# Kernel tuning notes

Measured on AMD Instinct MI355X. Metric: run time of the kernel, lower is better.

The kernel has to match this reference:

```python
import jax, jax.numpy as jnp
import numpy as np

B, L, D, H1, OUT, MAX_W = 16, 128, 768, 770, 40, 30


def _span_mask():
    # valid spans: i <= j and width < MAX_W (structured sparsity over the L x L grid)
    ii, jj = np.meshgrid(np.arange(L), np.arange(L), indexing='ij')
    return ((jj >= ii) & (jj - ii < MAX_W)).astype(np.int32)


def setup_inputs():
    key = jax.random.key(0)
    ks = jax.random.split(key, 5)
    hidden_states = jax.random.normal(ks[0], (B, L + 1, D), dtype=jnp.float32)
    rng = np.random.default_rng(0)
    starts = rng.integers(0, L - MAX_W, size=(B,))
    ends = starts + rng.integers(0, MAX_W, size=(B,))
    pred_spans = jnp.asarray(np.stack([starts, ends], axis=1), dtype=jnp.int32)
    span_mask = jnp.asarray(_span_mask())
    W1 = 0.02 * jax.random.normal(ks[1], (2 * D + 1, H1), dtype=jnp.float32)
    b1 = jax.random.normal(ks[2], (H1,), dtype=jnp.float32)
    W2 = 0.02 * jax.random.normal(ks[3], (H1, OUT), dtype=jnp.float32)
    b2 = jax.random.normal(ks[4], (OUT,), dtype=jnp.float32)
    return dict(hidden_states=hidden_states, pred_spans=pred_spans, token_num=L,
                span_available_indication_matrix=span_mask,
                W1=W1, b1=b1, W2=W2, b2=b2)


def reference(hidden_states, pred_spans, token_num, span_available_indication_matrix, W1, b1, W2, b2):
    # span mask is an integer constant -> resolve valid (i, j) pairs on host
    mask = np.asarray(span_available_indication_matrix)
    vi, vj = np.nonzero(mask == 1)            # [n_valid] each
    vi_j = jnp.asarray(vi)
    vj_j = jnp.asarray(vj)
    vecs = hidden_states[:, 1:token_num + 1, :]  # token t -> hidden[:, t+1, :], [B, L, D]
    xi = vecs[:, vi_j, :]                        # [B, n_valid, D] gather of span-start vecs
    xj = vecs[:, vj_j, :]                        # [B, n_valid, D] gather of span-end vecs
    # pred_indications: 2 if span == pred span; 1 if strictly inside it (i<=j); else 0
    s = pred_spans[:, 0:1]
    e = pred_spans[:, 1:2]
    i_ = vi_j[None, :]
    j_ = vj_j[None, :]
    exact = (i_ == s) & (j_ == e)
    inside = (i_ >= s) & (j_ <= e) & (i_ <= j_)
    ind = jnp.where(exact, 2.0, jnp.where(inside, 1.0, 0.0)).astype(hidden_states.dtype)  # [B, n_valid]
    # Linear over concat([xi, xj, ind]) expressed as split matmuls (avoids materializing concat)
    W1i, W1j, w1c = W1[:D], W1[D:2 * D], W1[2 * D]
    h = (jnp.einsum('bnd,dh->bnh', xi, W1i)
         + jnp.einsum('bnd,dh->bnh', xj, W1j)
         + ind[..., None] * w1c + b1)
    h = jax.nn.relu(h)
    logits = jnp.einsum('bnh,ho->bno', h, W2) + b2   # [B, n_valid, OUT]
    return jax.nn.log_softmax(logits, axis=-1)
```

## Files before the change

### kernel.cpp

```cpp
#include <hip/hip_runtime.h>
#include <math.h>

#define B_ 16
#define L_ 128
#define D_ 768
#define H1_ 770
#define OUT_ 40
#define NPAIRS 3405
#define NLOG 1540
#define YSB 1552
#define VOFFB 776
#define KPAD 800
#define W1TROWS 1600
#define NKS 25
#define NTILES 252
#define BSWZ_N (26 * 3 * 512)

#define NB_X 1536
#define NB_W 166
#define NB_T 1200
#define NB_A (NB_X + NB_W + NB_T)
#define NB_B 800
#define NB_C (NTILES * 16)

typedef __attribute__((ext_vector_type(8))) short bf16x8;
typedef __attribute__((ext_vector_type(8))) unsigned short u16x8;
typedef __attribute__((ext_vector_type(4))) float f32x4;
typedef __attribute__((ext_vector_type(4))) unsigned int u32x4;

__device__ inline unsigned short f2bf(float f) {
  unsigned int u = __builtin_bit_cast(unsigned int, f);
  u += 0x7fffu + ((u >> 16) & 1u);
  return (unsigned short)(u >> 16);
}
__device__ inline float bf2f(unsigned short x) {
  return __builtin_bit_cast(float, (unsigned int)x << 16);
}

#if __has_builtin(__builtin_amdgcn_cvt_pk_bf16_f32)
typedef __attribute__((ext_vector_type(2))) __bf16 bf16x2_t;
__device__ inline unsigned int pack_bf16(float lo, float hi) {
  bf16x2_t r = __builtin_amdgcn_cvt_pk_bf16_f32(lo, hi);
  return __builtin_bit_cast(unsigned int, r);
}
#else
__device__ inline unsigned int pack_bf16(float lo, float hi) {
  return (unsigned int)f2bf(lo) | ((unsigned int)f2bf(hi) << 16);
}
#endif

typedef const __attribute__((address_space(1))) void* gas_t;
typedef __attribute__((address_space(3))) void* las_t;
__device__ inline void gl2lds16(const void* g, void* l) {
  __builtin_amdgcn_global_load_lds((gas_t)g, (las_t)l, 16, 0, 0);
}

__device__ inline void tile_decode(int T, int& ti, int& d) {
  if (T < 216) { ti = T / 9; d = T - ti * 9; }
  else {
    int m = T - 216; int r = 24, w = 8;
    while (m >= w) { m -= w; --w; ++r; }
    ti = r; d = m;
  }
}
__device__ inline int pair_rank(int i, int j) {
  return (i < 99) ? i * 30 + (j - i)
                  : NPAIRS - (128 - i) * (129 - i) / 2 + (j - i);
}

__global__ __launch_bounds__(256) void prep_k(
    const float* __restrict__ hidden, const float* __restrict__ W1,
    const float* __restrict__ b1, const float* __restrict__ W2,
    unsigned short* __restrict__ Xb, unsigned short* __restrict__ W1T,
    unsigned short* __restrict__ Bswz, float* __restrict__ Cv)
{
  __shared__ float t[32][33];
  const int u = blockIdx.x;
  const int tid = threadIdx.x;

  if (u < NB_X) {
    int idx = u * 256 + tid;
    int m = idx / 192;
    int c = idx - m * 192;
    float4 f = *(const float4*)(hidden + (size_t)(m + (m >> 7) + 1) * D_ + c * 4);
    ushort4 o;
    o.x = f2bf(f.x); o.y = f2bf(f.y); o.z = f2bf(f.z); o.w = f2bf(f.w);
    *(ushort4*)(Xb + (size_t)m * D_ + c * 4) = o;
  } else if (u < NB_X + NB_W) {
    int idx = (u - NB_X) * 256 + tid;
    if (idx < BSWZ_N) {
      int ks = idx / 1536;
      int rem = idx - ks * 1536;
      int f = rem / 512;
      int l = (rem - f * 512) >> 3;
      int e = rem & 7;
      int n = f * 16 + (l & 15);
      int k = ks * 32 + (l >> 4) * 8 + e;
      float v = (n < OUT_ && k < H1_) ? W2[k * OUT_ + n] : 0.f;
      Bswz[idx] = f2bf(v);
    } else if (idx < BSWZ_N + 3 * KPAD) {
      int c = idx - BSWZ_N;
      int tt = c / KPAD, k = c - tt * KPAD;
      const float* w1c = W1 + 1536 * H1_;
      Cv[c] = (k < H1_) ? (b1[k] + (float)tt * w1c[k]) : 0.f;
    }
  } else {
    int bx = u - NB_X - NB_W;
    const int tx = tid & 31, ty = tid >> 5;
    const int n0 = (bx % 50) * 32, k0 = (bx / 50) * 32;
    #pragma unroll
    for (int r = 0; r < 4; ++r) {
      int k = k0 + ty + r * 8, n = n0 + tx;
      float v = 0.f;
      if (n < H1_)       v = W1[k * H1_ + n];
      else if (n < NLOG) v = W1[(D_ + k) * H1_ + (n - H1_)];
      t[ty + r * 8][tx] = v;
    }
    __syncthreads();
    #pragma unroll
    for (int r = 0; r < 4; ++r) {
      int n = n0 + ty + r * 8, k = k0 + tx;
      W1T[(size_t)n * D_ + k] = f2bf(t[tx][ty + r * 8]);
    }
  }
}

__global__ __launch_bounds__(256) void gemm_k(
    const unsigned short* __restrict__ Xb, const unsigned short* __restrict__ W1T,
    unsigned short* __restrict__ Yb)
{
  __shared__ unsigned short As[64][64];
  __shared__ unsigned short Bs[64][64];
  const int tid = threadIdx.x;
  const int lane = tid & 63, w = tid >> 6;
  const int lm = lane & 15, q = lane >> 4;
  const int xcd = blockIdx.x & 7;
  const int t = blockIdx.x >> 3;
  const int col0 = (t % 25) * 64;
  const int row0 = (xcd * 4 + t / 25) * 64;
  const int m0 = (w >> 1) * 32, n0 = (w & 1) * 32;

  const int srow = w * 16 + (lane >> 3);
  const int schunk = (((lane & 7) ^ ((lane >> 3) & 7))) * 8;
  const unsigned short* ga = Xb  + (size_t)(row0 + srow) * D_ + schunk;
  const unsigned short* gb = W1T + (size_t)(col0 + srow) * D_ + schunk;

  const int xs = lm & 7;

  f32x4 acc[2][2] = {};

  for (int k0 = 0; k0 < D_; k0 += 64) {
    gl2lds16(ga + k0,          &As[w * 16][0]);
    gl2lds16(ga + k0 + 8 * D_, &As[w * 16 + 8][0]);
    gl2lds16(gb + k0,          &Bs[w * 16][0]);
    gl2lds16(gb + k0 + 8 * D_, &Bs[w * 16 + 8][0]);
    __syncthreads();
    #pragma unroll
    for (int ks = 0; ks < 2; ++ks) {
      const int cc = ((ks * 4 + q) ^ xs) * 8;
      bf16x8 a0 = *(const bf16x8*)&As[m0 + lm]     [cc];
      bf16x8 a1 = *(const bf16x8*)&As[m0 + 16 + lm][cc];
      bf16x8 b0 = *(const bf16x8*)&Bs[n0 + lm]     [cc];
      bf16x8 b1 = *(const bf16x8*)&Bs[n0 + 16 + lm][cc];
      acc[0][0] = __builtin_amdgcn_mfma_f32_16x16x32_bf16(a0, b0, acc[0][0], 0, 0, 0);
      acc[0][1] = __builtin_amdgcn_mfma_f32_16x16x32_bf16(a0, b1, acc[0][1], 0, 0, 0);
      acc[1][0] = __builtin_amdgcn_mfma_f32_16x16x32_bf16(a1, b0, acc[1][0], 0, 0, 0);
      acc[1][1] = __builtin_amdgcn_mfma_f32_16x16x32_bf16(a1, b1, acc[1][1], 0, 0, 0);
    }
    __syncthreads();
  }

  #pragma unroll
  for (int ti = 0; ti < 2; ++ti) {
    #pragma unroll
    for (int tj = 0; tj < 2; ++tj) {
      int col = col0 + n0 + tj * 16 + lm;
      if (col >= NLOG) continue;
      int pc = (col < H1_) ? col : col + (VOFFB - H1_);
      #pragma unroll
      for (int r = 0; r < 4; ++r) {
        int row = row0 + m0 + ti * 16 + q * 4 + r;
        Yb[(size_t)row * YSB + pc] = f2bf(acc[ti][tj][r]);
      }
    }
  }
}

__global__ __launch_bounds__(64) void pair_k(
    const unsigned short* __restrict__ Yb, const int* __restrict__ spans,
    const unsigned short* __restrict__ Bswz, const float* __restrict__ Cv,
    const float* __restrict__ b2, float* __restrict__ out)
{
  const int tid = threadIdx.x;
  const int u = blockIdx.x;
  const int bb = u & 15;
  const int T = u >> 4;
  const int lm = tid & 15, q = tid >> 4;

  int ti, d;
  tile_decode(T, ti, d);
  const int i0 = ti * 4, j0 = (ti + d) * 4;

  const int ai = i0 + (lm & 3);
  const int aj = j0 + (lm >> 2);
  const int s = spans[2 * bb], e = spans[2 * bb + 1];
  const int ind = (ai == s && aj == e) ? 2 : ((ai >= s && aj <= e) ? 1 : 0);

  const unsigned short* uptr = Yb + (size_t)(bb * L_ + ai) * YSB + q * 8;
  const unsigned short* vptr = Yb + (size_t)(bb * L_ + aj) * YSB + VOFFB + q * 8;
  const float* cptr = Cv + ind * KPAD + q * 8;
  const unsigned short* bbase = Bswz + tid * 8;

  f32x4 acc0 = {}, acc1 = {}, acc2 = {};

  u16x8 uu0 = *(const u16x8*)(uptr);
  u16x8 vv0 = *(const u16x8*)(vptr);
  u16x8 uu1 = *(const u16x8*)(uptr + 32);
  u16x8 vv1 = *(const u16x8*)(vptr + 32);
  bf16x8 nb0 = *(const bf16x8*)(bbase + 0 * 512);
  bf16x8 nb1 = *(const bf16x8*)(bbase + 1 * 512);
  bf16x8 nb2 = *(const bf16x8*)(bbase + 2 * 512);

  #pragma unroll 5
  for (int ks = 0; ks < NKS; ++ks) {
    const int ko = ks * 32;
    u16x8 cu = uu0, cw = vv0;
    uu0 = uu1; vv0 = vv1;
    uu1 = *(const u16x8*)(uptr + ko + 64);
    vv1 = *(const u16x8*)(vptr + ko + 64);
    bf16x8 b0 = nb0, b1v = nb1, b2f = nb2;
    nb0 = *(const bf16x8*)(bbase + (size_t)(ks * 3 + 3) * 512);
    nb1 = *(const bf16x8*)(bbase + (size_t)(ks * 3 + 4) * 512);
    nb2 = *(const bf16x8*)(bbase + (size_t)(ks * 3 + 5) * 512);
    float4 c0 = *(const float4*)(cptr + ko);
    float4 c1 = *(const float4*)(cptr + ko + 4);
    float h0 = fmaxf(bf2f(cu[0]) + bf2f(cw[0]) + c0.x, 0.f);
    float h1 = fmaxf(bf2f(cu[1]) + bf2f(cw[1]) + c0.y, 0.f);
    float h2 = fmaxf(bf2f(cu[2]) + bf2f(cw[2]) + c0.z, 0.f);
    float h3 = fmaxf(bf2f(cu[3]) + bf2f(cw[3]) + c0.w, 0.f);
    float h4 = fmaxf(bf2f(cu[4]) + bf2f(cw[4]) + c1.x, 0.f);
    float h5 = fmaxf(bf2f(cu[5]) + bf2f(cw[5]) + c1.y, 0.f);
    float h6 = fmaxf(bf2f(cu[6]) + bf2f(cw[6]) + c1.z, 0.f);
    float h7 = fmaxf(bf2f(cu[7]) + bf2f(cw[7]) + c1.w, 0.f);
    u32x4 hp;
    hp[0] = pack_bf16(h0, h1);
    hp[1] = pack_bf16(h2, h3);
    hp[2] = pack_bf16(h4, h5);
    hp[3] = pack_bf16(h6, h7);
    bf16x8 a = __builtin_bit_cast(bf16x8, hp);
    acc0 = __builtin_amdgcn_mfma_f32_16x16x32_bf16(a, b0, acc0, 0, 0, 0);
    acc1 = __builtin_amdgcn_mfma_f32_16x16x32_bf16(a, b1v, acc1, 0, 0, 0);
    acc2 = __builtin_amdgcn_mfma_f32_16x16x32_bf16(a, b2f, acc2, 0, 0, 0);
  }

  const float b2v0 = b2[lm];
  const float b2v1 = b2[16 + lm];
  const float b2v2 = (lm < 8) ? b2[32 + lm] : 0.f;

  #pragma unroll
  for (int r = 0; r < 4; ++r) {
    float l0 = acc0[r] + b2v0;
    float l1 = acc1[r] + b2v1;
    float l2 = (lm < 8) ? (acc2[r] + b2v2) : -INFINITY;
    float mx = fmaxf(fmaxf(l0, l1), l2);
    mx = fmaxf(mx, __shfl_xor(mx, 1));
    mx = fmaxf(mx, __shfl_xor(mx, 2));
    mx = fmaxf(mx, __shfl_xor(mx, 4));
    mx = fmaxf(mx, __shfl_xor(mx, 8));
    float sm = expf(l0 - mx) + expf(l1 - mx) + ((lm < 8) ? expf(l2 - mx) : 0.f);
    sm += __shfl_xor(sm, 1);
    sm += __shfl_xor(sm, 2);
    sm += __shfl_xor(sm, 4);
    sm += __shfl_xor(sm, 8);
    float lsd = mx + logf(sm);

    int pi_ = i0 + r, pj_ = j0 + q;
    if (pj_ >= pi_ && (pj_ - pi_) < 30) {
      float* op = out + ((size_t)bb * NPAIRS + pair_rank(pi_, pj_)) * OUT_;
      op[lm]      = l0 - lsd;
      op[16 + lm] = l1 - lsd;
      if (lm < 8) op[32 + lm] = l2 - lsd;
    }
  }
}

extern "C" void kernel_launch(void* const* d_in, const int* in_sizes, int n_in,
                              void* d_out, int out_size, void* d_ws, size_t ws_size,
                              hipStream_t stream) {
  const float* hidden = (const float*)d_in[0];
  const int*   spans  = (const int*)d_in[1];
  const float* W1 = (const float*)d_in[4];
  const float* b1 = (const float*)d_in[5];
  const float* W2 = (const float*)d_in[6];
  const float* b2 = (const float*)d_in[7];
  float* out = (float*)d_out;

  char* base = (char*)d_ws;
  size_t off = 0;
  auto take = [&](size_t bytes) {
    char* p = base + off;
    off = (off + bytes + 255) & ~(size_t)255;
    return p;
  };
  unsigned short* Yb   = (unsigned short*)take((size_t)2049 * YSB * 2);
  unsigned short* Xb   = (unsigned short*)take((size_t)2048 * D_ * 2);
  unsigned short* W1T  = (unsigned short*)take((size_t)W1TROWS * D_ * 2);
  unsigned short* Bswz = (unsigned short*)take((size_t)BSWZ_N * 2);
  float*          Cv   = (float*)take((size_t)3 * KPAD * 4);

  prep_k<<<dim3(NB_A), 256, 0, stream>>>(hidden, W1, b1, W2, Xb, W1T, Bswz, Cv);
  gemm_k<<<dim3(NB_B), 256, 0, stream>>>(Xb, W1T, Yb);
  pair_k<<<dim3(NB_C), 64, 0, stream>>>(Yb, spans, Bswz, Cv, b2, out);
}
```

Measured before the change: 118.8 us.

## Fold b1 into GEMM epilogue, skip indicator loads, widen GEMM K-tile

```diff
diff --git a/kernel.cpp b/kernel.cpp
--- a/kernel.cpp
+++ b/kernel.cpp
@@ -32,9 +32,6 @@
   unsigned int u = __builtin_bit_cast(unsigned int, f);
   u += 0x7fffu + ((u >> 16) & 1u);
   return (unsigned short)(u >> 16);
-}
-__device__ inline float bf2f(unsigned short x) {
-  return __builtin_bit_cast(float, (unsigned int)x << 16);
 }
 
 #if __has_builtin(__builtin_amdgcn_cvt_pk_bf16_f32)
@@ -100,9 +97,12 @@
       Bswz[idx] = f2bf(v);
     } else if (idx < BSWZ_N + 3 * KPAD) {
       int c = idx - BSWZ_N;
-      int tt = c / KPAD, k = c - tt * KPAD;
+      int tt = c / KPAD, rem = c - tt * KPAD;
+      int g = rem >> 3, pos = rem & 7;
+      int m = (pos < 4) ? (pos * 2) : ((pos - 4) * 2 + 1);
+      int k = g * 8 + m;
       const float* w1c = W1 + 1536 * H1_;
-      Cv[c] = (k < H1_) ? (b1[k] + (float)tt * w1c[k]) : 0.f;
+      Cv[c] = (k < H1_) ? ((float)tt * w1c[k]) : 0.f;
     }
   } else {
     int bx = u - NB_X - NB_W;
@@ -127,10 +127,10 @@
 
 __global__ __launch_bounds__(256) void gemm_k(
     const unsigned short* __restrict__ Xb, const unsigned short* __restrict__ W1T,
-    unsigned short* __restrict__ Yb)
+    const float* __restrict__ b1, unsigned short* __restrict__ Yb)
 {
-  __shared__ unsigned short As[64][64];
-  __shared__ unsigned short Bs[64][64];
+  __shared__ unsigned short As[64][128];
+  __shared__ unsigned short Bs[64][128];
   const int tid = threadIdx.x;
   const int lane = tid & 63, w = tid >> 6;
   const int lm = lane & 15, q = lane >> 4;
@@ -140,47 +140,52 @@
   const int row0 = (xcd * 4 + t / 25) * 64;
   const int m0 = (w >> 1) * 32, n0 = (w & 1) * 32;
 
-  const int srow = w * 16 + (lane >> 3);
-  const int schunk = (((lane & 7) ^ ((lane >> 3) & 7))) * 8;
-  const unsigned short* ga = Xb  + (size_t)(row0 + srow) * D_ + schunk;
-  const unsigned short* gb = W1T + (size_t)(col0 + srow) * D_ + schunk;
-
-  const int xs = lm & 7;
+  const unsigned short* ga4[4];
+  const unsigned short* gb4[4];
+  #pragma unroll
+  for (int i = 0; i < 4; ++i) {
+    int srow = w * 16 + 4 * i + (lane >> 4);
+    int chunk = (lane & 15) ^ (srow & 15);
+    ga4[i] = Xb  + (size_t)(row0 + srow) * D_ + chunk * 8;
+    gb4[i] = W1T + (size_t)(col0 + srow) * D_ + chunk * 8;
+  }
 
   f32x4 acc[2][2] = {};
 
-  for (int k0 = 0; k0 < D_; k0 += 64) {
-    gl2lds16(ga + k0,          &As[w * 16][0]);
-    gl2lds16(ga + k0 + 8 * D_, &As[w * 16 + 8][0]);
-    gl2lds16(gb + k0,          &Bs[w * 16][0]);
-    gl2lds16(gb + k0 + 8 * D_, &Bs[w * 16 + 8][0]);
+  for (int k0 = 0; k0 < D_; k0 += 128) {
+    #pragma unroll
+    for (int i = 0; i < 4; ++i) {
+      gl2lds16(ga4[i] + k0, &As[w * 16 + 4 * i][0]);
+      gl2lds16(gb4[i] + k0, &Bs[w * 16 + 4 * i][0]);
+    }
     __syncthreads();
     #pragma unroll
-    for (int ks = 0; ks < 2; ++ks) {
-      const int cc = ((ks * 4 + q) ^ xs) * 8;
+    for (int ks = 0; ks < 4; ++ks) {
+      const int cc = (((ks * 4 + q) ^ lm)) * 8;
       bf16x8 a0 = *(const bf16x8*)&As[m0 + lm]     [cc];
       bf16x8 a1 = *(const bf16x8*)&As[m0 + 16 + lm][cc];
       bf16x8 b0 = *(const bf16x8*)&Bs[n0 + lm]     [cc];
-      bf16x8 b1 = *(const bf16x8*)&Bs[n0 + 16 + lm][cc];
+      bf16x8 b1v = *(const bf16x8*)&Bs[n0 + 16 + lm][cc];
       acc[0][0] = __builtin_amdgcn_mfma_f32_16x16x32_bf16(a0, b0, acc[0][0], 0, 0, 0);
-      acc[0][1] = __builtin_amdgcn_mfma_f32_16x16x32_bf16(a0, b1, acc[0][1], 0, 0, 0);
+      acc[0][1] = __builtin_amdgcn_mfma_f32_16x16x32_bf16(a0, b1v, acc[0][1], 0, 0, 0);
       acc[1][0] = __builtin_amdgcn_mfma_f32_16x16x32_bf16(a1, b0, acc[1][0], 0, 0, 0);
-      acc[1][1] = __builtin_amdgcn_mfma_f32_16x16x32_bf16(a1, b1, acc[1][1], 0, 0, 0);
+      acc[1][1] = __builtin_amdgcn_mfma_f32_16x16x32_bf16(a1, b1v, acc[1][1], 0, 0, 0);
     }
     __syncthreads();
   }
 
   #pragma unroll
-  for (int ti = 0; ti < 2; ++ti) {
-    #pragma unroll
-    for (int tj = 0; tj < 2; ++tj) {
-      int col = col0 + n0 + tj * 16 + lm;
-      if (col >= NLOG) continue;
-      int pc = (col < H1_) ? col : col + (VOFFB - H1_);
+  for (int tj = 0; tj < 2; ++tj) {
+    int col = col0 + n0 + tj * 16 + lm;
+    if (col >= NLOG) continue;
+    float badd = (col < H1_) ? b1[col] : 0.f;
+    int pc = (col < H1_) ? col : col + (VOFFB - H1_);
+    #pragma unroll
+    for (int ti = 0; ti < 2; ++ti) {
       #pragma unroll
       for (int r = 0; r < 4; ++r) {
         int row = row0 + m0 + ti * 16 + q * 4 + r;
-        Yb[(size_t)row * YSB + pc] = f2bf(acc[ti][tj][r]);
+        Yb[(size_t)row * YSB + pc] = f2bf(acc[ti][tj][r] + badd);
       }
     }
   }
@@ -205,6 +210,7 @@
   const int aj = j0 + (lm >> 2);
   const int s = spans[2 * bb], e = spans[2 * bb + 1];
   const int ind = (ai == s && aj == e) ? 2 : ((ai >= s && aj <= e) ? 1 : 0);
+  const bool withc = (__ballot(ind != 0) != 0ull);
 
   const unsigned short* uptr = Yb + (size_t)(bb * L_ + ai) * YSB + q * 8;
   const unsigned short* vptr = Yb + (size_t)(bb * L_ + aj) * YSB + VOFFB + q * 8;
@@ -212,46 +218,53 @@
   const unsigned short* bbase = Bswz + tid * 8;
 
   f32x4 acc0 = {}, acc1 = {}, acc2 = {};
-
-  u16x8 uu0 = *(const u16x8*)(uptr);
-  u16x8 vv0 = *(const u16x8*)(vptr);
-  u16x8 uu1 = *(const u16x8*)(uptr + 32);
-  u16x8 vv1 = *(const u16x8*)(vptr + 32);
-  bf16x8 nb0 = *(const bf16x8*)(bbase + 0 * 512);
-  bf16x8 nb1 = *(const bf16x8*)(bbase + 1 * 512);
-  bf16x8 nb2 = *(const bf16x8*)(bbase + 2 * 512);
-
-  #pragma unroll 5
-  for (int ks = 0; ks < NKS; ++ks) {
-    const int ko = ks * 32;
-    u16x8 cu = uu0, cw = vv0;
-    uu0 = uu1; vv0 = vv1;
-    uu1 = *(const u16x8*)(uptr + ko + 64);
-    vv1 = *(const u16x8*)(vptr + ko + 64);
-    bf16x8 b0 = nb0, b1v = nb1, b2f = nb2;
-    nb0 = *(const bf16x8*)(bbase + (size_t)(ks * 3 + 3) * 512);
-    nb1 = *(const bf16x8*)(bbase + (size_t)(ks * 3 + 4) * 512);
-    nb2 = *(const bf16x8*)(bbase + (size_t)(ks * 3 + 5) * 512);
-    float4 c0 = *(const float4*)(cptr + ko);
-    float4 c1 = *(const float4*)(cptr + ko + 4);
-    float h0 = fmaxf(bf2f(cu[0]) + bf2f(cw[0]) + c0.x, 0.f);
-    float h1 = fmaxf(bf2f(cu[1]) + bf2f(cw[1]) + c0.y, 0.f);
-    float h2 = fmaxf(bf2f(cu[2]) + bf2f(cw[2]) + c0.z, 0.f);
-    float h3 = fmaxf(bf2f(cu[3]) + bf2f(cw[3]) + c0.w, 0.f);
-    float h4 = fmaxf(bf2f(cu[4]) + bf2f(cw[4]) + c1.x, 0.f);
-    float h5 = fmaxf(bf2f(cu[5]) + bf2f(cw[5]) + c1.y, 0.f);
-    float h6 = fmaxf(bf2f(cu[6]) + bf2f(cw[6]) + c1.z, 0.f);
-    float h7 = fmaxf(bf2f(cu[7]) + bf2f(cw[7]) + c1.w, 0.f);
-    u32x4 hp;
-    hp[0] = pack_bf16(h0, h1);
-    hp[1] = pack_bf16(h2, h3);
-    hp[2] = pack_bf16(h4, h5);
-    hp[3] = pack_bf16(h6, h7);
-    bf16x8 a = __builtin_bit_cast(bf16x8, hp);
-    acc0 = __builtin_amdgcn_mfma_f32_16x16x32_bf16(a, b0, acc0, 0, 0, 0);
-    acc1 = __builtin_amdgcn_mfma_f32_16x16x32_bf16(a, b1v, acc1, 0, 0, 0);
-    acc2 = __builtin_amdgcn_mfma_f32_16x16x32_bf16(a, b2f, acc2, 0, 0, 0);
-  }
+  const f32x4 zero = {0.f, 0.f, 0.f, 0.f};
+
+  auto run = [&](bool usec) {
+    u16x8 uu0 = *(const u16x8*)(uptr);
+    u16x8 vv0 = *(const u16x8*)(vptr);
+    u16x8 uu1 = *(const u16x8*)(uptr + 32);
+    u16x8 vv1 = *(const u16x8*)(vptr + 32);
+    bf16x8 nb0 = *(const bf16x8*)(bbase + 0 * 512);
+    bf16x8 nb1 = *(const bf16x8*)(bbase + 1 * 512);
+    bf16x8 nb2 = *(const bf16x8*)(bbase + 2 * 512);
+
+    #pragma unroll 5
+    for (int ks = 0; ks < NKS; ++ks) {
+      const int ko = ks * 32;
+      u16x8 cu = uu0, cw = vv0;
+      uu0 = uu1; vv0 = vv1;
+      uu1 = *(const u16x8*)(uptr + ko + 64);
+      vv1 = *(const u16x8*)(vptr + ko + 64);
+      bf16x8 b0 = nb0, b1v = nb1, b2f = nb2;
+      nb0 = *(const bf16x8*)(bbase + (size_t)(ks * 3 + 3) * 512);
+      nb1 = *(const bf16x8*)(bbase + (size_t)(ks * 3 + 4) * 512);
+      nb2 = *(const bf16x8*)(bbase + (size_t)(ks * 3 + 5) * 512);
+
+      u32x4 ud = __builtin_bit_cast(u32x4, cu);
+      u32x4 vd = __builtin_bit_cast(u32x4, cw);
+      f32x4 slo = __builtin_bit_cast(f32x4, ud << 16)
+                + __builtin_bit_cast(f32x4, vd << 16);
+      f32x4 shi = __builtin_bit_cast(f32x4, ud & 0xffff0000u)
+                + __builtin_bit_cast(f32x4, vd & 0xffff0000u);
+      if (usec) {
+        slo += *(const f32x4*)(cptr + ko);
+        shi += *(const f32x4*)(cptr + ko + 4);
+      }
+      slo = __builtin_elementwise_max(slo, zero);
+      shi = __builtin_elementwise_max(shi, zero);
+      u32x4 hp;
+      hp[0] = pack_bf16(slo[0], shi[0]);
+      hp[1] = pack_bf16(slo[1], shi[1]);
+      hp[2] = pack_bf16(slo[2], shi[2]);
+      hp[3] = pack_bf16(slo[3], shi[3]);
+      bf16x8 a = __builtin_bit_cast(bf16x8, hp);
+      acc0 = __builtin_amdgcn_mfma_f32_16x16x32_bf16(a, b0, acc0, 0, 0, 0);
+      acc1 = __builtin_amdgcn_mfma_f32_16x16x32_bf16(a, b1v, acc1, 0, 0, 0);
+      acc2 = __builtin_amdgcn_mfma_f32_16x16x32_bf16(a, b2f, acc2, 0, 0, 0);
+    }
+  };
+  if (withc) run(true); else run(false);
 
   const float b2v0 = b2[lm];
   const float b2v1 = b2[16 + lm];
@@ -309,6 +322,6 @@
   float*          Cv   = (float*)take((size_t)3 * KPAD * 4);
 
   prep_k<<<dim3(NB_A), 256, 0, stream>>>(hidden, W1, b1, W2, Xb, W1T, Bswz, Cv);
-  gemm_k<<<dim3(NB_B), 256, 0, stream>>>(Xb, W1T, Yb);
+  gemm_k<<<dim3(NB_B), 256, 0, stream>>>(Xb, W1T, b1, Yb);
   pair_k<<<dim3(NB_C), 64, 0, stream>>>(Yb, spans, Bswz, Cv, b2, out);
 }
```

Measured after the change: 119.2 us. Within noise of the previous version (+0.3%).
